# Performance work log

Hardware: AMD Instinct MI355X
Metric: run time of the kernel (lower is better)

The kernel has to match this reference:

```python
import jax, jax.numpy as jnp
import numpy as np

B, S, E, H = 2, 2048, 1024, 16
D = E // H  # head_dim = 64
NEG = -1e10


def setup_inputs() -> dict:
    key = jax.random.key(0)
    ks = jax.random.split(key, 12)
    sc = 1.0 / np.sqrt(E)
    return {
        "query": jax.random.normal(ks[0], (B, S, E), jnp.float32),
        "key_": jax.random.normal(ks[1], (B, S, E), jnp.float32),
        "value": jax.random.normal(ks[2], (B, S, E), jnp.float32),
        "mask": jax.random.randint(ks[3], (B, S), 0, 2, jnp.int32),
        "Wq": jax.random.normal(ks[4], (E, E), jnp.float32) * sc,
        "bq": jnp.zeros((E,), jnp.float32),
        "Wk": jax.random.normal(ks[5], (E, E), jnp.float32) * sc,
        "bk": jnp.zeros((E,), jnp.float32),
        "Wv": jax.random.normal(ks[6], (E, E), jnp.float32) * sc,
        "bv": jnp.zeros((E,), jnp.float32),
        "Wo": jax.random.normal(ks[7], (E, E), jnp.float32) * sc,
        "bo": jnp.zeros((E,), jnp.float32),
    }


def reference(query, key_, value, mask, Wq, bq, Wk, bk, Wv, bv, Wo, bo):
    # Linear projections (torch Linear: x @ W^T + b)
    Q = (query @ Wq.T + bq).reshape(B, S, H, D)
    K = (key_ @ Wk.T + bk).reshape(B, S, H, D)
    V = (value @ Wv.T + bv).reshape(B, S, H, D)
    # [B, H, Sq, Sk] scores
    scores = jnp.einsum("bqhd,bkhd->bhqk", Q, K) / jnp.sqrt(jnp.float32(D))
    # Original sets rows of masked query positions AND columns of masked key
    # positions to -1e10 (set, not add; overlapping assignment is same value).
    pad = (mask == 0)  # [B, S]
    bad = pad[:, :, None] | pad[:, None, :]  # [B, Sq, Sk]
    scores = scores + jnp.where(bad, NEG, 0.0)[:, None, :, :]
    weights = jax.nn.softmax(scores, axis=-1)
    out = jnp.einsum("bhqk,bkhd->bqhd", weights, V).reshape(B, S, E)
    return out @ Wo.T + bo
```

## Files before the change

### kernel.cpp

```cpp
#include <hip/hip_runtime.h>

typedef __attribute__((ext_vector_type(4)))  float          f32x4;
typedef __attribute__((ext_vector_type(16))) float          f32x16;
typedef __attribute__((ext_vector_type(8)))  short          s16x8;
typedef __attribute__((ext_vector_type(4)))  unsigned short u16x4;
typedef __attribute__((ext_vector_type(8)))  unsigned short u16x8;

#define MFMA_BF16(a, b, c) __builtin_amdgcn_mfma_f32_16x16x32_bf16((a), (b), (c), 0, 0, 0)
#define MFMA32(a, b, c)    __builtin_amdgcn_mfma_f32_32x32x16_bf16((a), (b), (c), 0, 0, 0)

static constexpr int Bb = 2, Ss = 2048, Ee = 1024, Hh = 16, Dd = 64;
static constexpr size_t M4 = 4u * 1024 * 1024;
static constexpr size_t M1 = 1024 * 1024;

__device__ __forceinline__ unsigned short f2b(float f) {
    unsigned u = __builtin_bit_cast(unsigned, f);
    u += 0x7fffu + ((u >> 16) & 1u);
    return (unsigned short)(u >> 16);
}

__device__ __forceinline__ void gld_lds16(const unsigned short* g, unsigned short* l) {
    __builtin_amdgcn_global_load_lds(
        (const __attribute__((address_space(1))) unsigned int*)g,
        (__attribute__((address_space(3))) unsigned int*)l, 16, 0, 0);
}

struct CvtArgs { const float* src[7]; unsigned short* dst;
                 const int* mask; float* maskf; };

__global__ __launch_bounds__(256) void cvt_bf16(CvtArgs a)
{
    if (blockIdx.x == 8192) {
#pragma unroll
        for (int j = 0; j < 16; j++) {
            int idx = threadIdx.x + j * 256;
            a.maskf[idx] = a.mask[idx] ? 1.f : 0.f;
        }
        return;
    }
    size_t i = ((size_t)blockIdx.x * 256 + threadIdx.x) * 8;
    int seg; size_t off;
    if (i < 3 * M4) { seg = (int)(i / M4);     off = i % M4; }
    else            { size_t j = i - 3 * M4;
                      seg = 3 + (int)(j / M1); off = j % M1; }
    const float* s = a.src[seg] + off;
    f32x4 x0 = *(const f32x4*)s;
    f32x4 x1 = *(const f32x4*)(s + 4);
    u16x8 o = (u16x8){f2b(x0[0]), f2b(x0[1]), f2b(x0[2]), f2b(x0[3]),
                      f2b(x1[0]), f2b(x1[1]), f2b(x1[2]), f2b(x1[3])};
    *(u16x8*)(a.dst + i) = o;
}

template <int OUT_MODE>
__device__ __forceinline__ void gemm_bf16_body(const unsigned short* __restrict__ A,
                                               const unsigned short* __restrict__ W,
                                               const float* __restrict__ bias,
                                               void* __restrict__ Cv,
                                               int m0, int n0)
{
    __shared__ __align__(16) unsigned short Al[2][128 * 32];
    __shared__ __align__(16) unsigned short Bl[2][128 * 32];

    const int tid  = threadIdx.x;
    const int lane = tid & 63;
    const int wid  = tid >> 6;
    const int quad = lane >> 4;
    const int lr   = lane & 15;
    const int wr   = (wid >> 1) * 64;
    const int wc   = (wid & 1) * 64;

    const int srow = wid * 32 + (lane >> 2);
    const int sk8  = (lane & 3) * 8;
    const unsigned short* gA = A + (size_t)(m0 + srow) * 1024 + sk8;
    const unsigned short* gW = W + (size_t)(n0 + srow) * 1024 + sk8;
    const int swid = wid * 1024;

    f32x4 acc[4][4];
#pragma unroll
    for (int i = 0; i < 4; i++)
#pragma unroll
        for (int j = 0; j < 4; j++) acc[i][j] = (f32x4){0.f, 0.f, 0.f, 0.f};

    gld_lds16(gA,             &Al[0][swid]);
    gld_lds16(gA + 16 * 1024, &Al[0][swid + 512]);
    gld_lds16(gW,             &Bl[0][swid]);
    gld_lds16(gW + 16 * 1024, &Bl[0][swid + 512]);
    __syncthreads();

#pragma unroll 2
    for (int it = 0; it < 32; ++it) {
        const int cur = it & 1;
        if (it + 1 < 32) {
            const int ks  = (it + 1) * 32;
            const int nxt = cur ^ 1;
            gld_lds16(gA + ks,             &Al[nxt][swid]);
            gld_lds16(gA + ks + 16 * 1024, &Al[nxt][swid + 512]);
            gld_lds16(gW + ks,             &Bl[nxt][swid]);
            gld_lds16(gW + ks + 16 * 1024, &Bl[nxt][swid + 512]);
        }

        s16x8 af[4], bf[4];
#pragma unroll
        for (int t = 0; t < 4; t++) {
            af[t] = *(const s16x8*)&Al[cur][(wr + t * 16 + lr) * 32 + quad * 8];
            bf[t] = *(const s16x8*)&Bl[cur][(wc + t * 16 + lr) * 32 + quad * 8];
        }
#pragma unroll
        for (int mt = 0; mt < 4; mt++)
#pragma unroll
            for (int nt = 0; nt < 4; nt++)
                acc[mt][nt] = MFMA_BF16(af[mt], bf[nt], acc[mt][nt]);

        __syncthreads();
    }

#pragma unroll
    for (int mt = 0; mt < 4; mt++)
#pragma unroll
        for (int nt = 0; nt < 4; nt++) {
            int   col  = n0 + wc + nt * 16 + lr;
            float bcol = bias[col];
            int   rbase = m0 + wr + mt * 16 + quad * 4;
            if (OUT_MODE == 2) {
                int bb = rbase >> 11, s = rbase & 2047;
                u16x4 pk;
#pragma unroll
                for (int r = 0; r < 4; r++) pk[r] = f2b(acc[mt][nt][r] + bcol);
                *(u16x4*)&((unsigned short*)Cv)[((size_t)(bb * 1024 + col)) * 2048 + s] = pk;
            } else {
#pragma unroll
                for (int r = 0; r < 4; r++) {
                    float v = acc[mt][nt][r] + bcol;
                    if (OUT_MODE == 3) v *= 0.180336884f;
                    ((unsigned short*)Cv)[(size_t)(rbase + r) * 1024 + col] = f2b(v);
                }
            }
        }
}

struct GArgs {
    const unsigned short* A[3];
    const unsigned short* W[3];
    const float* bias[3];
    unsigned short* C[3];
};

__global__ __launch_bounds__(256) void proj_gemm(GArgs ga)
{
    const int id  = blockIdx.x;
    const int xcd = id & 7;
    const int t   = id >> 3;
    const int z   = t >> 5;
    const int tt  = t & 31;
    const int n0  = (tt & 7) * 128;
    const int m0  = (xcd * 4 + (tt >> 3)) * 128;

    if (z == 2)      gemm_bf16_body<2>(ga.A[2], ga.W[2], ga.bias[2], ga.C[2], m0, n0);
    else if (z == 1) gemm_bf16_body<1>(ga.A[1], ga.W[1], ga.bias[1], ga.C[1], m0, n0);
    else             gemm_bf16_body<3>(ga.A[0], ga.W[0], ga.bias[0], ga.C[0], m0, n0);
}

__global__ __launch_bounds__(256)
void out_gemm(const unsigned short* __restrict__ A,
              const unsigned short* __restrict__ W,
              const float* __restrict__ bias,
              float* __restrict__ C)
{
    __shared__ __align__(16) unsigned short Al[2][128 * 32];
    __shared__ __align__(16) unsigned short Bl[2][64 * 32];

    const int id  = blockIdx.x;
    const int xcd = id & 7;
    const int t   = id >> 3;
    const int n0  = (t & 15) * 64;
    const int m0  = (xcd * 4 + (t >> 4)) * 128;

    const int tid  = threadIdx.x;
    const int lane = tid & 63;
    const int wid  = tid >> 6;
    const int quad = lane >> 4;
    const int lr   = lane & 15;
    const int wr   = (wid >> 1) * 64;
    const int wc   = (wid & 1) * 32;

    const int srowA = wid * 32 + (lane >> 2);
    const int srowW = wid * 16 + (lane >> 2);
    const int sk8   = (lane & 3) * 8;
    const unsigned short* gA = A + (size_t)(m0 + srowA) * 1024 + sk8;
    const unsigned short* gW = W + (size_t)(n0 + srowW) * 1024 + sk8;
    const int swidA = wid * 1024;
    const int swidW = wid * 512;

    f32x4 acc[4][2];
#pragma unroll
    for (int i = 0; i < 4; i++)
#pragma unroll
        for (int j = 0; j < 2; j++) acc[i][j] = (f32x4){0.f, 0.f, 0.f, 0.f};

    gld_lds16(gA,             &Al[0][swidA]);
    gld_lds16(gA + 16 * 1024, &Al[0][swidA + 512]);
    gld_lds16(gW,             &Bl[0][swidW]);
    __syncthreads();

#pragma unroll 2
    for (int it = 0; it < 32; ++it) {
        const int cur = it & 1;
        if (it + 1 < 32) {
            const int ks  = (it + 1) * 32;
            const int nxt = cur ^ 1;
            gld_lds16(gA + ks,             &Al[nxt][swidA]);
            gld_lds16(gA + ks + 16 * 1024, &Al[nxt][swidA + 512]);
            gld_lds16(gW + ks,             &Bl[nxt][swidW]);
        }

        s16x8 af[4], bf[2];
#pragma unroll
        for (int mt = 0; mt < 4; mt++)
            af[mt] = *(const s16x8*)&Al[cur][(wr + mt * 16 + lr) * 32 + quad * 8];
#pragma unroll
        for (int nt = 0; nt < 2; nt++)
            bf[nt] = *(const s16x8*)&Bl[cur][(wc + nt * 16 + lr) * 32 + quad * 8];
#pragma unroll
        for (int mt = 0; mt < 4; mt++)
#pragma unroll
            for (int nt = 0; nt < 2; nt++)
                acc[mt][nt] = MFMA_BF16(af[mt], bf[nt], acc[mt][nt]);

        __syncthreads();
    }

#pragma unroll
    for (int mt = 0; mt < 4; mt++)
#pragma unroll
        for (int nt = 0; nt < 2; nt++) {
            int   col  = n0 + wc + nt * 16 + lr;
            float bcol = bias[col];
            int   rbase = m0 + wr + mt * 16 + quad * 4;
#pragma unroll
            for (int r = 0; r < 4; r++)
                C[(size_t)(rbase + r) * 1024 + col] = acc[mt][nt][r] + bcol;
        }
}

__global__ __launch_bounds__(256)
void flash_attn(const unsigned short* __restrict__ Q,
                const unsigned short* __restrict__ K,
                const unsigned short* __restrict__ Vt,
                const float* __restrict__ maskf,
                unsigned short* __restrict__ O)
{
    constexpr int   ST  = 76;
    constexpr float EPS = 9.31322575e-10f;
    __shared__ __align__(16) unsigned short Kl[64 * ST];
    __shared__ __align__(16) unsigned short Vl[64 * ST];
    __shared__ __align__(16) unsigned short Pl[64 * ST];
    __shared__ float lsq[4][32];

    const int id    = blockIdx.x;
    const int xcd   = id & 7;
    const int local = id >> 3;
    const int pair  = xcd * 4 + (local >> 5);
    const int b     = pair >> 4;
    const int h     = pair & 15;
    const int q0    = (local & 31) * 64;

    const int tid  = threadIdx.x;
    const int lane = tid & 63;
    const int wid  = tid >> 6;
    const int l31  = lane & 31;
    const int hl   = lane >> 5;
    const int qh   = wid & 1;
    const int kh   = wid >> 1;

    const unsigned short* qg =
        Q + (size_t)(b * 2048 + q0 + qh * 32 + l31) * 1024 + h * 64 + hl * 8;
    s16x8 qf[4];
#pragma unroll
    for (int db = 0; db < 4; db++) qf[db] = *(const s16x8*)(qg + db * 16);

    const float  mq  = maskf[b * 2048 + q0 + qh * 32 + l31];
    const float* mkp = maskf + b * 2048;

    const int lk = (tid >> 3) * ST + (tid & 7) * 8;
    const unsigned short* gK = K  + (size_t)(b * 2048 + (tid >> 3)) * 1024 + h * 64 + (tid & 7) * 8;
    const unsigned short* gV = Vt + (size_t)(b * 1024 + h * 64 + (tid >> 3)) * 2048 + (tid & 7) * 8;

    float  lsum = 0.f;
    f32x16 accO = (f32x16){0.f,0.f,0.f,0.f,0.f,0.f,0.f,0.f,
                           0.f,0.f,0.f,0.f,0.f,0.f,0.f,0.f};

    for (int kt = 0; kt < 2048; kt += 64) {
        __syncthreads();
        *(u16x8*)&Kl[lk]           = *(const u16x8*)(gK + (size_t)kt * 1024);
        *(u16x8*)&Kl[lk + 32 * ST] = *(const u16x8*)(gK + (size_t)(kt + 32) * 1024);
        *(u16x8*)&Vl[lk]           = *(const u16x8*)(gV + kt);
        *(u16x8*)&Vl[lk + 32 * ST] = *(const u16x8*)(gV + kt + (size_t)32 * 2048);
        __syncthreads();

        f32x16 st = (f32x16){0.f,0.f,0.f,0.f,0.f,0.f,0.f,0.f,
                             0.f,0.f,0.f,0.f,0.f,0.f,0.f,0.f};
#pragma unroll
        for (int db = 0; db < 4; db++) {
            s16x8 kf = *(const s16x8*)&Kl[(kh * 32 + l31) * ST + db * 16 + hl * 8];
            st = MFMA32(kf, qf[db], st);
        }
#pragma unroll
        for (int rq = 0; rq < 4; rq++) {
            int   kb = 4 * hl + 8 * rq;
            f32x4 m4 = *(const f32x4*)&mkp[kt + kh * 32 + kb];
            unsigned u[4];
#pragma unroll
            for (int r = 0; r < 4; r++) {
                float e = __builtin_amdgcn_exp2f(st[rq * 4 + r]);
                float p = e * (m4[r] * mq) + EPS;
                lsum += p;
                u[r] = __builtin_bit_cast(unsigned, p) + 0x8000u;
            }
            uint2 w;
            w.x = __builtin_amdgcn_perm(u[1], u[0], 0x07060302u);
            w.y = __builtin_amdgcn_perm(u[3], u[2], 0x07060302u);
            *(uint2*)&Pl[(qh * 32 + l31) * ST + kh * 32 + kb] = w;
        }
        __syncthreads();

#pragma unroll
        for (int ks = 0; ks < 4; ks++) {
            s16x8 pf = *(const s16x8*)&Pl[(qh * 32 + l31) * ST + ks * 16 + hl * 8];
            s16x8 vf = *(const s16x8*)&Vl[(kh * 32 + l31) * ST + ks * 16 + hl * 8];
            accO = MFMA32(pf, vf, accO);
        }
    }

    lsum += __shfl_xor(lsum, 32, 64);
    lsq[wid][l31] = lsum;
    __syncthreads();

#pragma unroll
    for (int rq = 0; rq < 4; rq++) {
        int   qr = 4 * hl + 8 * rq;
        f32x4 lA = *(const f32x4*)&lsq[qh][qr];
        f32x4 lB = *(const f32x4*)&lsq[qh + 2][qr];
#pragma unroll
        for (int r = 0; r < 4; r++) {
            float val = accO[rq * 4 + r] * __builtin_amdgcn_rcpf(lA[r] + lB[r]);
            O[(size_t)(b * 2048 + q0 + qh * 32 + qr + r) * 1024 + h * 64 +
              kh * 32 + l31] = f2b(val);
        }
    }
}

extern "C" void kernel_launch(void* const* d_in, const int* in_sizes, int n_in,
                              void* d_out, int out_size, void* d_ws, size_t ws_size,
                              hipStream_t stream)
{
    const float* query = (const float*)d_in[0];
    const float* key_  = (const float*)d_in[1];
    const float* value = (const float*)d_in[2];
    const int*   mask  = (const int*)d_in[3];
    const float* Wq    = (const float*)d_in[4];
    const float* bq    = (const float*)d_in[5];
    const float* Wk    = (const float*)d_in[6];
    const float* bk    = (const float*)d_in[7];
    const float* Wv    = (const float*)d_in[8];
    const float* bv    = (const float*)d_in[9];
    const float* Wo    = (const float*)d_in[10];
    const float* bo    = (const float*)d_in[11];
    float* out = (float*)d_out;

    unsigned short* cvt = (unsigned short*)d_ws;
    unsigned short* Aq  = cvt;
    unsigned short* Ak  = cvt + M4;
    unsigned short* Av  = cvt + 2 * M4;
    unsigned short* Wqb = cvt + 3 * M4;
    unsigned short* Wkb = Wqb + M1;
    unsigned short* Wvb = Wkb + M1;
    unsigned short* Wob = Wvb + M1;
    unsigned short* Qb  = Wob + M1;
    unsigned short* Kb  = Qb + M4;
    unsigned short* Vt  = Kb + M4;
    unsigned short* Ab  = Vt + M4;
    float*          mkf = (float*)(Ab + M4);

    CvtArgs ca;
    ca.src[0] = query; ca.src[1] = key_; ca.src[2] = value;
    ca.src[3] = Wq; ca.src[4] = Wk; ca.src[5] = Wv; ca.src[6] = Wo;
    ca.dst = cvt; ca.mask = mask; ca.maskf = mkf;
    cvt_bf16<<<dim3(8193), 256, 0, stream>>>(ca);

    GArgs ga;
    ga.A[0] = Aq;  ga.A[1] = Ak;  ga.A[2] = Av;
    ga.W[0] = Wqb; ga.W[1] = Wkb; ga.W[2] = Wvb;
    ga.bias[0] = bq; ga.bias[1] = bk; ga.bias[2] = bv;
    ga.C[0] = Qb; ga.C[1] = Kb; ga.C[2] = Vt;
    proj_gemm<<<dim3(768), 256, 0, stream>>>(ga);

    flash_attn<<<dim3(1024), 256, 0, stream>>>(Qb, Kb, Vt, mkf, Ab);
    out_gemm<<<dim3(512), 256, 0, stream>>>(Ab, Wob, bo, out);
}
```

Before: 268.1 us.

## Replace double-buffered GEMM prefetch with single-stage 64-wide K tiles

Both projection GEMM kernels drop their ping-pong prefetch pipeline. Each iteration now loads a 64-wide K slice into both LDS buffers, waits at a barrier, then runs the MFMAs over both halves. This halves the number of loop iterations and barriers and simplifies the loop. In exchange, global-to-LDS loads no longer overlap with compute, so memory latency is exposed on every iteration.

Result: faster. 255.7 us (-4.6%).

```diff
diff --git a/kernel.cpp b/kernel.cpp
--- a/kernel.cpp
+++ b/kernel.cpp
@@ -81,37 +81,32 @@
 #pragma unroll
         for (int j = 0; j < 4; j++) acc[i][j] = (f32x4){0.f, 0.f, 0.f, 0.f};
 
-    gld_lds16(gA,             &Al[0][swid]);
-    gld_lds16(gA + 16 * 1024, &Al[0][swid + 512]);
-    gld_lds16(gW,             &Bl[0][swid]);
-    gld_lds16(gW + 16 * 1024, &Bl[0][swid + 512]);
-    __syncthreads();
-
-#pragma unroll 2
-    for (int it = 0; it < 32; ++it) {
-        const int cur = it & 1;
-        if (it + 1 < 32) {
-            const int ks  = (it + 1) * 32;
-            const int nxt = cur ^ 1;
-            gld_lds16(gA + ks,             &Al[nxt][swid]);
-            gld_lds16(gA + ks + 16 * 1024, &Al[nxt][swid + 512]);
-            gld_lds16(gW + ks,             &Bl[nxt][swid]);
-            gld_lds16(gW + ks + 16 * 1024, &Bl[nxt][swid + 512]);
-        }
-
-        s16x8 af[4], bf[4];
-#pragma unroll
-        for (int t = 0; t < 4; t++) {
-            af[t] = *(const s16x8*)&Al[cur][(wr + t * 16 + lr) * 32 + quad * 8];
-            bf[t] = *(const s16x8*)&Bl[cur][(wc + t * 16 + lr) * 32 + quad * 8];
-        }
-#pragma unroll
-        for (int mt = 0; mt < 4; mt++)
-#pragma unroll
-            for (int nt = 0; nt < 4; nt++)
-                acc[mt][nt] = MFMA_BF16(af[mt], bf[nt], acc[mt][nt]);
-
-        __syncthreads();
+    for (int ks = 0; ks < 1024; ks += 64) {
+        __syncthreads();
+        gld_lds16(gA + ks,                  &Al[0][swid]);
+        gld_lds16(gA + ks + 16 * 1024,      &Al[0][swid + 512]);
+        gld_lds16(gA + ks + 32,             &Al[1][swid]);
+        gld_lds16(gA + ks + 32 + 16 * 1024, &Al[1][swid + 512]);
+        gld_lds16(gW + ks,                  &Bl[0][swid]);
+        gld_lds16(gW + ks + 16 * 1024,      &Bl[0][swid + 512]);
+        gld_lds16(gW + ks + 32,             &Bl[1][swid]);
+        gld_lds16(gW + ks + 32 + 16 * 1024, &Bl[1][swid + 512]);
+        __syncthreads();
+
+#pragma unroll
+        for (int kk = 0; kk < 2; kk++) {
+            s16x8 af[4], bf[4];
+#pragma unroll
+            for (int t = 0; t < 4; t++) {
+                af[t] = *(const s16x8*)&Al[kk][(wr + t * 16 + lr) * 32 + quad * 8];
+                bf[t] = *(const s16x8*)&Bl[kk][(wc + t * 16 + lr) * 32 + quad * 8];
+            }
+#pragma unroll
+            for (int mt = 0; mt < 4; mt++)
+#pragma unroll
+                for (int nt = 0; nt < 4; nt++)
+                    acc[mt][nt] = MFMA_BF16(af[mt], bf[nt], acc[mt][nt]);
+        }
     }
 
 #pragma unroll
@@ -197,36 +192,31 @@
 #pragma unroll
         for (int j = 0; j < 2; j++) acc[i][j] = (f32x4){0.f, 0.f, 0.f, 0.f};
 
-    gld_lds16(gA,             &Al[0][swidA]);
-    gld_lds16(gA + 16 * 1024, &Al[0][swidA + 512]);
-    gld_lds16(gW,             &Bl[0][swidW]);
-    __syncthreads();
-
-#pragma unroll 2
-    for (int it = 0; it < 32; ++it) {
-        const int cur = it & 1;
-        if (it + 1 < 32) {
-            const int ks  = (it + 1) * 32;
-            const int nxt = cur ^ 1;
-            gld_lds16(gA + ks,             &Al[nxt][swidA]);
-            gld_lds16(gA + ks + 16 * 1024, &Al[nxt][swidA + 512]);
-            gld_lds16(gW + ks,             &Bl[nxt][swidW]);
-        }
-
-        s16x8 af[4], bf[2];
-#pragma unroll
-        for (int mt = 0; mt < 4; mt++)
-            af[mt] = *(const s16x8*)&Al[cur][(wr + mt * 16 + lr) * 32 + quad * 8];
-#pragma unroll
-        for (int nt = 0; nt < 2; nt++)
-            bf[nt] = *(const s16x8*)&Bl[cur][(wc + nt * 16 + lr) * 32 + quad * 8];
-#pragma unroll
-        for (int mt = 0; mt < 4; mt++)
+    for (int ks = 0; ks < 1024; ks += 64) {
+        __syncthreads();
+        gld_lds16(gA + ks,                  &Al[0][swidA]);
+        gld_lds16(gA + ks + 16 * 1024,      &Al[0][swidA + 512]);
+        gld_lds16(gA + ks + 32,             &Al[1][swidA]);
+        gld_lds16(gA + ks + 32 + 16 * 1024, &Al[1][swidA + 512]);
+        gld_lds16(gW + ks,                  &Bl[0][swidW]);
+        gld_lds16(gW + ks + 32,             &Bl[1][swidW]);
+        __syncthreads();
+
+#pragma unroll
+        for (int kk = 0; kk < 2; kk++) {
+            s16x8 af[4], bf[2];
+#pragma unroll
+            for (int mt = 0; mt < 4; mt++)
+                af[mt] = *(const s16x8*)&Al[kk][(wr + mt * 16 + lr) * 32 + quad * 8];
 #pragma unroll
             for (int nt = 0; nt < 2; nt++)
-                acc[mt][nt] = MFMA_BF16(af[mt], bf[nt], acc[mt][nt]);
-
-        __syncthreads();
+                bf[nt] = *(const s16x8*)&Bl[kk][(wc + nt * 16 + lr) * 32 + quad * 8];
+#pragma unroll
+            for (int mt = 0; mt < 4; mt++)
+#pragma unroll
+                for (int nt = 0; nt < 2; nt++)
+                    acc[mt][nt] = MFMA_BF16(af[mt], bf[nt], acc[mt][nt]);
+        }
     }
 
 #pragma unroll
```
